# Kernel tuning notes

Hardware: AMD Instinct MI355X
Metric: run time of the kernel (lower is better)

## Reference

```python
import jax, jax.numpy as jnp
import numpy as np

N_NODES = 100000
N_EDGES = 1000000
N_FEAT = 136
HIDDEN = 64
N_CLASSES = 2
NUM_GRAPHS = 512


def setup_inputs() -> dict:
    key = jax.random.key(0)
    ks = jax.random.split(key, 8)
    x = jax.random.normal(ks[0], (N_NODES, N_FEAT), dtype=jnp.float32)
    edge_index = jax.random.randint(ks[1], (2, N_EDGES), 0, N_NODES, dtype=jnp.int64)
    batch = jnp.sort(jax.random.randint(ks[2], (N_NODES,), 0, NUM_GRAPHS, dtype=jnp.int64))
    W1 = jax.random.normal(ks[3], (N_FEAT, HIDDEN), dtype=jnp.float32) * (1.0 / np.sqrt(N_FEAT))
    b1 = jnp.zeros((HIDDEN,), dtype=jnp.float32)
    W2 = jax.random.normal(ks[4], (HIDDEN, HIDDEN), dtype=jnp.float32) * (1.0 / np.sqrt(HIDDEN))
    b2 = jnp.zeros((HIDDEN,), dtype=jnp.float32)
    Wout = jax.random.normal(ks[5], (HIDDEN, N_CLASSES), dtype=jnp.float32) * (1.0 / np.sqrt(HIDDEN))
    bout = jnp.zeros((N_CLASSES,), dtype=jnp.float32)
    return {"x": x, "edge_index": edge_index, "batch": batch,
            "W1": W1, "b1": b1, "W2": W2, "b2": b2, "Wout": Wout, "bout": bout}


def _gcn_conv(x, src, dst, W, b, n_nodes):
    # GCNConv: D^{-1/2} (A+I) D^{-1/2} X W + b (self-loops already appended in src/dst)
    h = x @ W                                           # [N, out]
    ones = jnp.ones(src.shape, dtype=h.dtype)
    deg = jax.ops.segment_sum(ones, dst, num_segments=n_nodes)  # in-degree incl. self-loop
    dinv = jnp.where(deg > 0, jax.lax.rsqrt(deg), 0.0)
    norm = dinv[src] * dinv[dst]                        # [E]
    msg = h[src] * norm[:, None]                        # gather + normalize
    out = jax.ops.segment_sum(msg, dst, num_segments=n_nodes)   # scatter-add
    return out + b


def reference(x, edge_index, batch, W1, b1, W2, b2, Wout, bout):
    n = x.shape[0]
    loops = jnp.arange(n, dtype=edge_index.dtype)
    src = jnp.concatenate([edge_index[0], loops])
    dst = jnp.concatenate([edge_index[1], loops])

    h = jax.nn.relu(_gcn_conv(x, src, dst, W1, b1, n))
    # dropout p=0.5 is identity in eval mode
    h = jax.nn.relu(_gcn_conv(h, src, dst, W2, b2, n))

    # global_mean_pool over batch segments
    sums = jax.ops.segment_sum(h, batch, num_segments=NUM_GRAPHS)       # [G, H]
    counts = jax.ops.segment_sum(jnp.ones((n,), h.dtype), batch, num_segments=NUM_GRAPHS)
    pooled = sums / jnp.maximum(counts, 1.0)[:, None]

    return pooled @ Wout + bout                                         # [G, C]
```

## Files before the change

kernel.cpp:

```cpp
#include <hip/hip_runtime.h>
#include <hip/hip_bf16.h>

#define N_NODES   100000
#define N_EDGES   1000000
#define N_FEAT    136
#define HIDDEN    64
#define N_CLASSES 2
#define NUM_GRAPHS 512

#define NP_PAD    100352
#define SCAN_BLKS 98

#define EPW       128
#define NWAVE     7813
#define E_PAD     (NWAVE * EPW)
#define SEG_BLOCKS ((NWAVE + 3) / 4)

#define K1_4 (N_FEAT / 4)
#define K1PAD 160
#define K2PAD 72

#define NB_SC   ((N_EDGES / 4 + 255) / 256)
#define NB_MM   ((N_NODES + 63) / 64)

#define NCH   32
#define CHK   (N_EDGES / NCH)
#define NRG   8
#define RNG   (N_NODES / NRG)
#define NP1   (NCH * NRG)
#define NGB   3
#define FUSED_GRID (NP1 + NGB + NB_MM)

typedef unsigned short ushort_t;
typedef unsigned char u8_t;
typedef __attribute__((ext_vector_type(8))) short bf16x8;
typedef __attribute__((ext_vector_type(4))) float f32x4;
typedef __attribute__((ext_vector_type(4))) int i32x4;
typedef __attribute__((ext_vector_type(4))) unsigned short u16x4;

__device__ __forceinline__ ushort_t f2b(float v) {
    unsigned b = __float_as_uint(v);
    return (ushort_t)((b + 0x7FFF + ((b >> 16) & 1)) >> 16);
}
__device__ __forceinline__ float b2f(ushort_t u) {
    return __uint_as_float(((unsigned)u) << 16);
}
__device__ __forceinline__ unsigned pack2(float a, float b) {
    return (unsigned)f2b(a) | ((unsigned)f2b(b) << 16);
}

__global__ __launch_bounds__(256) void fused_csr_mm1_kernel(
        const int* __restrict__ dst,
        ushort_t* __restrict__ rank, u8_t* __restrict__ chunkcnt,
        const int* __restrict__ batch, int* __restrict__ gstart,
        const float* __restrict__ x, const float* __restrict__ W1,
        ushort_t* __restrict__ tpb) {
    __shared__ __align__(16) char smem_u[RNG * 4];
    int t = threadIdx.x;
    int bid = blockIdx.x;

    if (bid < NP1) {
        int* lh = (int*)smem_u;
        int c = bid >> 3, r = bid & 7;
        for (int i = t; i < RNG; i += 256) lh[i] = 0;
        __syncthreads();
        int e0 = c * CHK;
        int lo = r * RNG;
        for (int i = t; i < CHK; i += 256) {
            int e = e0 + i;
            int d = __builtin_nontemporal_load(&dst[e]) - lo;
            if ((unsigned)d < (unsigned)RNG) {
                int rk = atomicAdd(&lh[d], 1);
                rank[e] = (ushort_t)rk;
            }
        }
        __syncthreads();
        u8_t* cc = &chunkcnt[(size_t)c * N_NODES + lo];
        for (int i = t; i < RNG; i += 256) cc[i] = (u8_t)lh[i];
        return;
    }

    if (bid < NP1 + NGB) {
        int g = (bid - NP1) * 256 + t;
        if (g <= NUM_GRAPHS) {
            int lo = 0, hi = N_NODES;
            while (lo < hi) {
                int mid = (lo + hi) >> 1;
                if (batch[mid] < g) lo = mid + 1; else hi = mid;
            }
            gstart[g] = lo;
        }
        return;
    }

    ushort_t* wtb = (ushort_t*)smem_u;
    int mb = bid - NP1 - NGB;
    int n0 = mb * 64;
    {
        for (int i = t; i < N_FEAT * HIDDEN; i += 256) {
            int n = i & 63, k = i >> 6;
            wtb[n * K1PAD + k] = f2b(W1[i]);
        }
        for (int i = t; i < 64 * 12; i += 256) {
            int n = i / 12, c = i % 12;
            *(unsigned*)&wtb[n * K1PAD + N_FEAT + 2 * c] = 0;
        }
    }
    __syncthreads();
    int w = t >> 6, lane = t & 63;
    int quad = lane >> 4, l16 = lane & 15;
    int an = n0 + w * 16 + l16; if (an >= N_NODES) an = N_NODES - 1;
    const f32x4* xr = (const f32x4*)(x + (long long)an * N_FEAT);
    f32x4 acc[4] = {{0,0,0,0},{0,0,0,0},{0,0,0,0},{0,0,0,0}};
#pragma unroll
    for (int kc = 0; kc < K1PAD / 32; ++kc) {
        int k0 = kc * 32 + quad * 8;
        bf16x8 a = {0, 0, 0, 0, 0, 0, 0, 0};
        if (k0 < N_FEAT) {
            f32x4 u0 = __builtin_nontemporal_load(&xr[kc * 8 + quad * 2]);
            f32x4 u1 = __builtin_nontemporal_load(&xr[kc * 8 + quad * 2 + 1]);
            union { bf16x8 v; unsigned u[4]; } cv;
            cv.u[0] = pack2(u0.x, u0.y);
            cv.u[1] = pack2(u0.z, u0.w);
            cv.u[2] = pack2(u1.x, u1.y);
            cv.u[3] = pack2(u1.z, u1.w);
            a = cv.v;
        }
#pragma unroll
        for (int nt = 0; nt < 4; ++nt) {
            bf16x8 b = *(const bf16x8*)&wtb[(nt * 16 + l16) * K1PAD + kc * 32 + quad * 8];
            acc[nt] = __builtin_amdgcn_mfma_f32_16x16x32_bf16(a, b, acc[nt], 0, 0, 0);
        }
    }
#pragma unroll
    for (int r = 0; r < 4; ++r) {
        int nl = w * 16 + quad * 4 + r;
        int node = n0 + nl;
        if (node < N_NODES) {
#pragma unroll
            for (int nt = 0; nt < 4; ++nt)
                tpb[node * 64 + nt * 16 + l16] = f2b(acc[nt][r]);
        }
    }
}

__global__ __launch_bounds__(256) void colscan_kernel(u8_t* __restrict__ chunkcnt,
                                                      int* __restrict__ cnt) {
    int d = blockIdx.x * 256 + threadIdx.x;
    if (d >= N_NODES) return;
    int s = 0;
#pragma unroll
    for (int c = 0; c < NCH; ++c) {
        size_t idx = (size_t)c * N_NODES + d;
        int v = chunkcnt[idx];
        chunkcnt[idx] = (u8_t)s;
        s += v;
    }
    cnt[d] = s;
}

__global__ __launch_bounds__(256) void scan1_kernel(const int* __restrict__ cnt,
                                                    int* __restrict__ row_ptr,
                                                    int* __restrict__ partials) {
    __shared__ int sd[256];
    int b = blockIdx.x, t = threadIdx.x;
    int i0 = b * 1024 + t * 4;
    int c0 = (i0 + 0 < N_NODES) ? cnt[i0 + 0] : 0;
    int c1 = (i0 + 1 < N_NODES) ? cnt[i0 + 1] : 0;
    int c2 = (i0 + 2 < N_NODES) ? cnt[i0 + 2] : 0;
    int c3 = (i0 + 3 < N_NODES) ? cnt[i0 + 3] : 0;
    int tsum = c0 + c1 + c2 + c3;
    sd[t] = tsum;
    __syncthreads();
    for (int off = 1; off < 256; off <<= 1) {
        int v = (t >= off) ? sd[t - off] : 0;
        __syncthreads();
        sd[t] += v;
        __syncthreads();
    }
    int excl = sd[t] - tsum;
    row_ptr[i0 + 0] = excl;
    row_ptr[i0 + 1] = excl + c0;
    row_ptr[i0 + 2] = excl + c0 + c1;
    row_ptr[i0 + 3] = excl + c0 + c1 + c2;
    if (t == 255) partials[b] = sd[255];
}

__global__ __launch_bounds__(128) void scan2_kernel(int* __restrict__ partials) {
    __shared__ int sd[128];
    int t = threadIdx.x;
    int v = (t < SCAN_BLKS) ? partials[t] : 0;
    sd[t] = v;
    __syncthreads();
    for (int off = 1; off < 128; off <<= 1) {
        int u = (t >= off) ? sd[t - off] : 0;
        __syncthreads();
        sd[t] += u;
        __syncthreads();
    }
    partials[t] = sd[t] - v;
}

__global__ __launch_bounds__(256) void scan3_kernel(int* __restrict__ row_ptr,
                                                    const int* __restrict__ cnt,
                                                    const int* __restrict__ partials,
                                                    int* __restrict__ dst_sorted,
                                                    int* __restrict__ csr_src,
                                                    float* __restrict__ dinv) {
    int i = blockIdx.x * 256 + threadIdx.x;
    if (i < N_NODES) {
        int v = row_ptr[i] + partials[i >> 10];
        int deg = cnt[i];
        row_ptr[i] = v;
        dinv[i] = rsqrtf((float)(deg + 1));
        for (int j = v; j < v + deg; ++j) dst_sorted[j] = i;
    }
    if (i == N_NODES) {
        row_ptr[N_NODES] = N_EDGES;
        for (int j = N_EDGES; j < E_PAD; ++j) {
            dst_sorted[j] = N_NODES;
            csr_src[j] = 0;
        }
    }
}

__global__ __launch_bounds__(256) void scatter_kernel(const int* __restrict__ src,
                                                      const int* __restrict__ dst,
                                                      const ushort_t* __restrict__ rank,
                                                      const u8_t* __restrict__ chunkpre,
                                                      const int* __restrict__ row_ptr,
                                                      int* __restrict__ csr_src) {
    int e0 = (blockIdx.x * 256 + threadIdx.x) * 4;
    if (e0 >= N_EDGES) return;
    i32x4 s4 = __builtin_nontemporal_load((const i32x4*)&src[e0]);
    i32x4 d4 = __builtin_nontemporal_load((const i32x4*)&dst[e0]);
    u16x4 r4 = *(const u16x4*)&rank[e0];
    int c0 = (e0 + 0) / CHK, c1 = (e0 + 1) / CHK;
    int c2 = (e0 + 2) / CHK, c3 = (e0 + 3) / CHK;
    int p0 = row_ptr[d4.x] + (int)chunkpre[(size_t)c0 * N_NODES + d4.x] + (int)r4.x;
    int p1 = row_ptr[d4.y] + (int)chunkpre[(size_t)c1 * N_NODES + d4.y] + (int)r4.y;
    int p2 = row_ptr[d4.z] + (int)chunkpre[(size_t)c2 * N_NODES + d4.z] + (int)r4.z;
    int p3 = row_ptr[d4.w] + (int)chunkpre[(size_t)c3 * N_NODES + d4.w] + (int)r4.w;
    csr_src[p0] = s4.x;
    csr_src[p1] = s4.y;
    csr_src[p2] = s4.z;
    csr_src[p3] = s4.w;
}

__global__ __launch_bounds__(256) void mm2_kernel(float* __restrict__ agg,
                                                  ushort_t* __restrict__ tpb,
                                                  const float* __restrict__ W2,
                                                  const float* __restrict__ dinv,
                                                  const float* __restrict__ bias) {
    __shared__ ushort_t hsb[64 * K2PAD];
    __shared__ ushort_t wtb[64 * K2PAD];
    __shared__ float    dsv[64];
    __shared__ float    bsv[64];
    int t = threadIdx.x;
    int n0 = blockIdx.x * 64;
    if (t < 64) {
        int n = n0 + t; if (n >= N_NODES) n = N_NODES - 1;
        dsv[t] = dinv[n];
        bsv[t] = bias[t];
    }
    __syncthreads();
    {
        for (int i = t; i < HIDDEN * HIDDEN; i += 256) {
            int n = i & 63, k = i >> 6;
            wtb[n * K2PAD + k] = f2b(W2[i]);
        }
        for (int i = t; i < 64 * 4; i += 256) {
            int n = i / 4, c = i % 4;
            *(unsigned*)&wtb[n * K2PAD + HIDDEN + 2 * c] = 0;
        }
        for (int i = t; i < 64 * 16; i += 256) {
            int r = i >> 4, c = i & 15;
            int n_raw = n0 + r;
            int n = (n_raw < N_NODES) ? n_raw : N_NODES - 1;
            float4 va = ((const float4*)agg)[n * 16 + c];
            uint2 ut = *(const uint2*)&tpb[n * 64 + c * 4];
            float di = dsv[r];
            float s0 = b2f((ushort_t)(ut.x & 0xffff)) * di;
            float s1 = b2f((ushort_t)(ut.x >> 16)) * di;
            float s2 = b2f((ushort_t)(ut.y & 0xffff)) * di;
            float s3 = b2f((ushort_t)(ut.y >> 16)) * di;
            float h0 = fmaxf(fmaf(va.x + s0, di, bsv[c * 4 + 0]), 0.f);
            float h1 = fmaxf(fmaf(va.y + s1, di, bsv[c * 4 + 1]), 0.f);
            float h2 = fmaxf(fmaf(va.z + s2, di, bsv[c * 4 + 2]), 0.f);
            float h3 = fmaxf(fmaf(va.w + s3, di, bsv[c * 4 + 3]), 0.f);
            *(uint2*)&hsb[r * K2PAD + 4 * c] = make_uint2(pack2(h0, h1), pack2(h2, h3));
            if (n_raw < N_NODES)
                ((float4*)agg)[n * 16 + c] = make_float4(0.f, 0.f, 0.f, 0.f);
        }
        for (int i = t; i < 64 * 4; i += 256) {
            int r = i / 4, c = i % 4;
            *(unsigned*)&hsb[r * K2PAD + HIDDEN + 2 * c] = 0;
        }
    }
    __syncthreads();
    int w = t >> 6, lane = t & 63;
    int quad = lane >> 4, l16 = lane & 15;
    f32x4 acc[4] = {{0,0,0,0},{0,0,0,0},{0,0,0,0},{0,0,0,0}};
#pragma unroll
    for (int kc = 0; kc < 2; ++kc) {
        bf16x8 a = *(const bf16x8*)&hsb[(w * 16 + l16) * K2PAD + kc * 32 + quad * 8];
#pragma unroll
        for (int nt = 0; nt < 4; ++nt) {
            bf16x8 b = *(const bf16x8*)&wtb[(nt * 16 + l16) * K2PAD + kc * 32 + quad * 8];
            acc[nt] = __builtin_amdgcn_mfma_f32_16x16x32_bf16(a, b, acc[nt], 0, 0, 0);
        }
    }
#pragma unroll
    for (int r = 0; r < 4; ++r) {
        int nl = w * 16 + quad * 4 + r;
        int node = n0 + nl;
        if (node < N_NODES) {
            float di = dsv[nl];
#pragma unroll
            for (int nt = 0; nt < 4; ++nt)
                tpb[node * 64 + nt * 16 + l16] = f2b(acc[nt][r] * di);
        }
    }
}

template<bool SCALE_SRC>
__global__ __launch_bounds__(256, 4) void edge_seg_kernel(const int* __restrict__ csr_src,
                                                          const int* __restrict__ dst_sorted,
                                                          const ushort_t* __restrict__ tpb,
                                                          const float* __restrict__ dinv,
                                                          float* __restrict__ agg) {
    int lane = threadIdx.x & 63;
    int wid  = (blockIdx.x * 256 + threadIdx.x) >> 6;
    if (wid >= NWAVE) return;
    int e0 = wid * EPW;

    int sv0 = csr_src[e0 + lane],      sv1 = csr_src[e0 + 64 + lane];
    int dv0 = dst_sorted[e0 + lane],   dv1 = dst_sorted[e0 + 64 + lane];

    float acc = 0.0f;
    int dprev = __builtin_amdgcn_readlane(dv0, 0);
    int nflush = 0;
#pragma unroll
    for (int j = 0; j < 8; ++j) {
        int svj = (j < 4) ? sv0 : sv1;
        int dvj = (j < 4) ? dv0 : dv1;
        int base = (j * 16) & 63;
        int ss[16], dd[16];
#pragma unroll
        for (int k = 0; k < 16; ++k) {
            ss[k] = __builtin_amdgcn_readlane(svj, base + k);
            dd[k] = __builtin_amdgcn_readlane(dvj, base + k);
        }
        float vv[16];
#pragma unroll
        for (int k = 0; k < 16; ++k) {
            float v = b2f(tpb[ss[k] * 64 + lane]);
            if (SCALE_SRC) v *= dinv[ss[k]];
            vv[k] = v;
        }
#pragma unroll
        for (int k = 0; k < 16; ++k) {
            if (dd[k] != dprev) {
                if (nflush == 0) atomicAdd(&agg[dprev * 64 + lane], acc);
                else             agg[dprev * 64 + lane] = acc;
                ++nflush;
                acc = 0.0f;
                dprev = dd[k];
            }
            acc += vv[k];
        }
    }
    atomicAdd(&agg[dprev * 64 + lane], acc);
}

__global__ __launch_bounds__(256) void gpool_kernel(const float* __restrict__ agg,
                                                    const ushort_t* __restrict__ tpb,
                                                    const float* __restrict__ dinv,
                                                    const float* __restrict__ bias,
                                                    const int* __restrict__ gstart,
                                                    const float* __restrict__ Wout,
                                                    const float* __restrict__ bout,
                                                    float* __restrict__ out) {
    __shared__ float red[4][64];
    int lane = threadIdx.x & 63;
    int w = threadIdx.x >> 6;
    int g = blockIdx.x;
    int s = gstart[g], e = gstart[g + 1];
    float b = bias[lane];
    float acc = 0.0f;
    for (int n = s + w; n < e; n += 4) {
        int idx = n * 64 + lane;
        acc += fmaxf(fmaf(agg[idx] + b2f(tpb[idx]), dinv[n], b), 0.0f);
    }
    red[w][lane] = acc;
    __syncthreads();
    if (threadIdx.x < 64) {
        float tot = red[0][lane] + red[1][lane] + red[2][lane] + red[3][lane];
        float p = tot / fmaxf((float)(e - s), 1.0f);
        float c0 = p * Wout[lane * N_CLASSES + 0];
        float c1 = p * Wout[lane * N_CLASSES + 1];
#pragma unroll
        for (int off = 32; off > 0; off >>= 1) {
            c0 += __shfl_down(c0, off);
            c1 += __shfl_down(c1, off);
        }
        if (lane == 0) {
            out[g * N_CLASSES + 0] = c0 + bout[0];
            out[g * N_CLASSES + 1] = c1 + bout[1];
        }
    }
}

extern "C" void kernel_launch(void* const* d_in, const int* in_sizes, int n_in,
                              void* d_out, int out_size, void* d_ws, size_t ws_size,
                              hipStream_t stream) {
    const float* x     = (const float*)d_in[0];
    const int*   ei    = (const int*)d_in[1];
    const int*   batch = (const int*)d_in[2];
    const float* W1    = (const float*)d_in[3];
    const float* b1    = (const float*)d_in[4];
    const float* W2    = (const float*)d_in[5];
    const float* b2    = (const float*)d_in[6];
    const float* Wout  = (const float*)d_in[7];
    const float* bout  = (const float*)d_in[8];
    float* out = (float*)d_out;

    const int* src = ei;
    const int* dst = ei + N_EDGES;

    char* p = (char*)d_ws;
    int*      row_ptr   = (int*)p;      p += (NP_PAD + 256) * sizeof(int);
    int*      cnt       = (int*)p;      p += NP_PAD * sizeof(int);
    int*      partials  = (int*)p;      p += 256 * sizeof(int);
    int*      gstart    = (int*)p;      p += (NUM_GRAPHS + 64) * sizeof(int);
    int*      csr_src   = (int*)p;      p += (size_t)E_PAD * sizeof(int);
    int*      dst_sorted= (int*)p;      p += (size_t)E_PAD * sizeof(int);
    float*    dinv      = (float*)p;    p += NP_PAD * sizeof(float);
    ushort_t* tpb       = (ushort_t*)p; p += (size_t)N_NODES * HIDDEN * sizeof(ushort_t);
    float*    agg       = (float*)p;    p += (size_t)(N_NODES + 1) * HIDDEN * sizeof(float);
    ushort_t* rank16    = (ushort_t*)agg;
    u8_t*     chunkcnt  = (u8_t*)agg + (size_t)E_PAD * sizeof(ushort_t);

    fused_csr_mm1_kernel<<<FUSED_GRID, 256, 0, stream>>>(dst, rank16, chunkcnt,
                                                         batch, gstart,
                                                         x, W1, tpb);
    colscan_kernel<<<(N_NODES + 255) / 256, 256, 0, stream>>>(chunkcnt, cnt);
    scan1_kernel<<<SCAN_BLKS, 256, 0, stream>>>(cnt, row_ptr, partials);
    scan2_kernel<<<1, 128, 0, stream>>>(partials);
    scan3_kernel<<<NP_PAD / 256 + 1, 256, 0, stream>>>(row_ptr, cnt, partials,
                                                       dst_sorted, csr_src, dinv);
    scatter_kernel<<<NB_SC, 256, 0, stream>>>(src, dst, rank16, chunkcnt,
                                              row_ptr, csr_src);

    hipMemsetAsync(agg, 0, (size_t)(N_NODES + 1) * HIDDEN * sizeof(float), stream);

    edge_seg_kernel<true><<<SEG_BLOCKS, 256, 0, stream>>>(csr_src, dst_sorted,
                                                          tpb, dinv, agg);

    mm2_kernel<<<NB_MM, 256, 0, stream>>>(agg, tpb, W2, dinv, b1);
    edge_seg_kernel<false><<<SEG_BLOCKS, 256, 0, stream>>>(csr_src, dst_sorted,
                                                           tpb, dinv, agg);

    gpool_kernel<<<NUM_GRAPHS, 256, 0, stream>>>(agg, tpb, dinv, b2, gstart,
                                                 Wout, bout, out);
}
```

Measured before the change: 306.6 us.

## Pack per-chunk histograms into byte counters and split CSR build from MM1

```diff
diff --git a/kernel.cpp b/kernel.cpp
--- a/kernel.cpp
+++ b/kernel.cpp
@@ -23,13 +23,13 @@
 #define NB_SC   ((N_EDGES / 4 + 255) / 256)
 #define NB_MM   ((N_NODES + 63) / 64)
 
-#define NCH   32
+#define NCH   125
 #define CHK   (N_EDGES / NCH)
-#define NRG   8
-#define RNG   (N_NODES / NRG)
-#define NP1   (NCH * NRG)
+#define NRG   2
+#define RNG   50000
+#define HWORDS (RNG / 4)
+#define NHB   (NCH * NRG)
 #define NGB   3
-#define FUSED_GRID (NP1 + NGB + NB_MM)
 
 typedef unsigned short ushort_t;
 typedef unsigned char u8_t;
@@ -49,39 +49,16 @@
     return (unsigned)f2b(a) | ((unsigned)f2b(b) << 16);
 }
 
-__global__ __launch_bounds__(256) void fused_csr_mm1_kernel(
+__global__ __launch_bounds__(256) void hist8_kernel(
         const int* __restrict__ dst,
         ushort_t* __restrict__ rank, u8_t* __restrict__ chunkcnt,
-        const int* __restrict__ batch, int* __restrict__ gstart,
-        const float* __restrict__ x, const float* __restrict__ W1,
-        ushort_t* __restrict__ tpb) {
-    __shared__ __align__(16) char smem_u[RNG * 4];
+        const int* __restrict__ batch, int* __restrict__ gstart) {
+    __shared__ unsigned lh[HWORDS];
     int t = threadIdx.x;
     int bid = blockIdx.x;
 
-    if (bid < NP1) {
-        int* lh = (int*)smem_u;
-        int c = bid >> 3, r = bid & 7;
-        for (int i = t; i < RNG; i += 256) lh[i] = 0;
-        __syncthreads();
-        int e0 = c * CHK;
-        int lo = r * RNG;
-        for (int i = t; i < CHK; i += 256) {
-            int e = e0 + i;
-            int d = __builtin_nontemporal_load(&dst[e]) - lo;
-            if ((unsigned)d < (unsigned)RNG) {
-                int rk = atomicAdd(&lh[d], 1);
-                rank[e] = (ushort_t)rk;
-            }
-        }
-        __syncthreads();
-        u8_t* cc = &chunkcnt[(size_t)c * N_NODES + lo];
-        for (int i = t; i < RNG; i += 256) cc[i] = (u8_t)lh[i];
-        return;
-    }
-
-    if (bid < NP1 + NGB) {
-        int g = (bid - NP1) * 256 + t;
+    if (bid >= NHB) {
+        int g = (bid - NHB) * 256 + t;
         if (g <= NUM_GRAPHS) {
             int lo = 0, hi = N_NODES;
             while (lo < hi) {
@@ -93,9 +70,31 @@
         return;
     }
 
-    ushort_t* wtb = (ushort_t*)smem_u;
-    int mb = bid - NP1 - NGB;
-    int n0 = mb * 64;
+    int c = bid >> 1, r = bid & 1;
+    for (int i = t; i < HWORDS; i += 256) lh[i] = 0;
+    __syncthreads();
+    int e0 = c * CHK;
+    int lo = r * RNG;
+    for (int i = t; i < CHK; i += 256) {
+        int e = e0 + i;
+        int d = __builtin_nontemporal_load(&dst[e]) - lo;
+        if ((unsigned)d < (unsigned)RNG) {
+            unsigned w = (unsigned)d >> 2, sh = ((unsigned)d & 3u) * 8u;
+            unsigned old = atomicAdd(&lh[w], 1u << sh);
+            rank[e] = (ushort_t)((old >> sh) & 0xffu);
+        }
+    }
+    __syncthreads();
+    unsigned* cc = (unsigned*)&chunkcnt[(size_t)c * N_NODES + lo];
+    for (int i = t; i < HWORDS; i += 256) cc[i] = lh[i];
+}
+
+__global__ __launch_bounds__(256) void mm1_kernel(const float* __restrict__ x,
+                                                  const float* __restrict__ W1,
+                                                  ushort_t* __restrict__ tpb) {
+    __shared__ ushort_t wtb[64 * K1PAD];
+    int t = threadIdx.x;
+    int n0 = blockIdx.x * 64;
     {
         for (int i = t; i < N_FEAT * HIDDEN; i += 256) {
             int n = i & 63, k = i >> 6;
@@ -149,7 +148,7 @@
     int d = blockIdx.x * 256 + threadIdx.x;
     if (d >= N_NODES) return;
     int s = 0;
-#pragma unroll
+#pragma unroll 5
     for (int c = 0; c < NCH; ++c) {
         size_t idx = (size_t)c * N_NODES + d;
         int v = chunkcnt[idx];
@@ -235,12 +234,12 @@
     i32x4 s4 = __builtin_nontemporal_load((const i32x4*)&src[e0]);
     i32x4 d4 = __builtin_nontemporal_load((const i32x4*)&dst[e0]);
     u16x4 r4 = *(const u16x4*)&rank[e0];
-    int c0 = (e0 + 0) / CHK, c1 = (e0 + 1) / CHK;
-    int c2 = (e0 + 2) / CHK, c3 = (e0 + 3) / CHK;
-    int p0 = row_ptr[d4.x] + (int)chunkpre[(size_t)c0 * N_NODES + d4.x] + (int)r4.x;
-    int p1 = row_ptr[d4.y] + (int)chunkpre[(size_t)c1 * N_NODES + d4.y] + (int)r4.y;
-    int p2 = row_ptr[d4.z] + (int)chunkpre[(size_t)c2 * N_NODES + d4.z] + (int)r4.z;
-    int p3 = row_ptr[d4.w] + (int)chunkpre[(size_t)c3 * N_NODES + d4.w] + (int)r4.w;
+    int c = e0 / CHK;
+    const u8_t* cp = &chunkpre[(size_t)c * N_NODES];
+    int p0 = row_ptr[d4.x] + (int)cp[d4.x] + (int)r4.x;
+    int p1 = row_ptr[d4.y] + (int)cp[d4.y] + (int)r4.y;
+    int p2 = row_ptr[d4.z] + (int)cp[d4.z] + (int)r4.z;
+    int p3 = row_ptr[d4.w] + (int)cp[d4.w] + (int)r4.w;
     csr_src[p0] = s4.x;
     csr_src[p1] = s4.y;
     csr_src[p2] = s4.z;
@@ -438,12 +437,12 @@
     float*    dinv      = (float*)p;    p += NP_PAD * sizeof(float);
     ushort_t* tpb       = (ushort_t*)p; p += (size_t)N_NODES * HIDDEN * sizeof(ushort_t);
     float*    agg       = (float*)p;    p += (size_t)(N_NODES + 1) * HIDDEN * sizeof(float);
-    ushort_t* rank16    = (ushort_t*)agg;
-    u8_t*     chunkcnt  = (u8_t*)agg + (size_t)E_PAD * sizeof(ushort_t);
-
-    fused_csr_mm1_kernel<<<FUSED_GRID, 256, 0, stream>>>(dst, rank16, chunkcnt,
-                                                         batch, gstart,
-                                                         x, W1, tpb);
+    ushort_t* rank16    = (ushort_t*)p; p += (size_t)E_PAD * sizeof(ushort_t);
+    u8_t*     chunkcnt  = (u8_t*)agg;
+
+    hist8_kernel<<<NHB + NGB, 256, 0, stream>>>(dst, rank16, chunkcnt,
+                                                batch, gstart);
+    mm1_kernel<<<NB_MM, 256, 0, stream>>>(x, W1, tpb);
     colscan_kernel<<<(N_NODES + 255) / 256, 256, 0, stream>>>(chunkcnt, cnt);
     scan1_kernel<<<SCAN_BLKS, 256, 0, stream>>>(cnt, row_ptr, partials);
     scan2_kernel<<<1, 128, 0, stream>>>(partials);
```

Measured after the change: 290.3 us. 1.06x faster.
